# Performance work log

Hardware: AMD Instinct MI355X
Metric: run time of the kernel (lower is better)

The kernel has to match this reference:

```python
import jax, jax.numpy as jnp
import numpy as np

B, N, H = 4, 256, 128
T = 8  # triplet hidden width


def _linear_init(key, fan_in, fan_out):
    s = 1.0 / np.sqrt(fan_in)
    kw, kb = jax.random.split(key)
    W = jax.random.uniform(kw, (fan_in, fan_out), minval=-s, maxval=s, dtype=jnp.float32)
    b = jax.random.uniform(kb, (fan_out,), minval=-s, maxval=s, dtype=jnp.float32)
    return W, b


def setup_inputs() -> dict:
    key = jax.random.key(0)
    ks = jax.random.split(key, 16)
    inp = {
        "node_embeddings": jax.random.normal(ks[0], (B, N, H), dtype=jnp.float32),
        "edge_embeddings": jax.random.normal(ks[1], (B, N, H), dtype=jnp.float32),
        "graph_embeddings": jax.random.normal(ks[2], (B, H), dtype=jnp.float32),
        "previous_hidden": jax.random.normal(ks[3], (B, N, H), dtype=jnp.float32),
    }
    # message MLP: (z_i 2H, z_j 2H, edge_j H, graph H) = 6H -> H -> H -> H
    inp["Wm1"], inp["bm1"] = _linear_init(ks[4], 6 * H, H)
    inp["Wm2"], inp["bm2"] = _linear_init(ks[5], H, H)
    inp["Wm3"], inp["bm3"] = _linear_init(ks[6], H, H)
    # gate MLP: (z 2H, m H, edge H, graph H) = 5H -> H -> H (sigmoid)
    inp["Wg1"], inp["bg1"] = _linear_init(ks[7], 5 * H, H)
    inp["Wg2"], inp["bg2"] = _linear_init(ks[8], H, H)
    # readout: (z 2H, m H) = 3H -> H
    inp["Wr"], inp["br"] = _linear_init(ks[9], 3 * H, H)
    # triplet MLP: (node_j H, node_k H, node H, edge 3H, graph H) = 7H -> 8 (relu)
    inp["Wt1"], inp["bt1"] = _linear_init(ks[10], 7 * H, T)
    # triplet edge readout: 8 -> H
    inp["Wt2"], inp["bt2"] = _linear_init(ks[11], T, H)
    # layer norm params
    inp["gamma"] = jnp.ones((H,), dtype=jnp.float32)
    inp["beta"] = jnp.zeros((H,), dtype=jnp.float32)
    return inp


def reference(node_embeddings, edge_embeddings, graph_embeddings, previous_hidden,
              Wm1, bm1, Wm2, bm2, Wm3, bm3,
              Wg1, bg1, Wg2, bg2, Wr, br,
              Wt1, bt1, Wt2, bt2, gamma, beta):
    h = node_embeddings.shape[-1]
    z = jnp.concatenate([node_embeddings, previous_hidden], axis=-1)  # [B,N,2H]

    # ---- pairwise messages: decompose first linear so the 6H-wide concat is never built ----
    W_zi, W_zj = Wm1[: 2 * h], Wm1[2 * h: 4 * h]
    W_e, W_g = Wm1[4 * h: 5 * h], Wm1[5 * h:]
    u = z @ W_zi + (graph_embeddings @ W_g)[:, None, :] + bm1   # per-i part [B,N,H]
    v = z @ W_zj + edge_embeddings @ W_e                        # per-j part [B,N,H]
    h1 = jax.nn.relu(u[:, :, None, :] + v[:, None, :, :])       # [B,Ni,Nj,H]
    h2 = jax.nn.relu(h1 @ Wm2 + bm2)
    msgs = h2 @ Wm3 + bm3                                       # [B,Ni,Nj,H]
    m = jnp.max(msgs, axis=2)                                   # max over j -> [B,N,H]

    gb = jnp.broadcast_to(graph_embeddings[:, None, :], node_embeddings.shape)
    gate_in = jnp.concatenate([z, m, edge_embeddings, gb], axis=-1)  # [B,N,5H]
    g = jax.nn.sigmoid(jax.nn.relu(gate_in @ Wg1 + bg1) @ Wg2 + bg2)
    h_i = jnp.concatenate([z, m], axis=-1) @ Wr + br
    h_g = g * h_i + (1.0 - g) * previous_hidden

    # ---- triplet messages ----
    # pre-activation is separable over (j, k, i), so max over the N^2 (k,j) pairs
    # equals per-channel max_j + max_k (relu is monotone, max commutes with it).
    Wt_j, Wt_k, Wt_n = Wt1[:h], Wt1[h: 2 * h], Wt1[2 * h: 3 * h]
    Wt_e = Wt1[3 * h: 4 * h] + Wt1[4 * h: 5 * h] + Wt1[5 * h: 6 * h]
    Wt_g = Wt1[6 * h:]
    a_j = node_embeddings @ Wt_j   # [B,N,8]
    a_k = node_embeddings @ Wt_k   # [B,N,8]
    c = node_embeddings @ Wt_n + edge_embeddings @ Wt_e + (graph_embeddings @ Wt_g)[:, None, :] + bt1
    t_max = jax.nn.relu(c + jnp.max(a_j, axis=1, keepdims=True) + jnp.max(a_k, axis=1, keepdims=True))
    h_ij = t_max @ Wt2 + bt2       # [B,N,H]

    # ---- layer norm on gated hidden ----
    mu = jnp.mean(h_g, axis=-1, keepdims=True)
    var = jnp.mean(jnp.square(h_g - mu), axis=-1, keepdims=True)
    h_norm = (h_g - mu) * jax.lax.rsqrt(var + 1e-5) * gamma + beta
    return (h_norm, h_ij)
```

## Files before the change

### kernel.cpp

```cpp
#include <hip/hip_runtime.h>
#include <hip/hip_bf16.h>

typedef unsigned short u16;
typedef float f32x4 __attribute__((ext_vector_type(4)));
typedef short s16x8 __attribute__((ext_vector_type(8)));

#define MFMA16(a,b,c) __builtin_amdgcn_mfma_f32_16x16x32_bf16((a),(b),(c),0,0,0)

static __device__ __forceinline__ u16 f2bf(float x){
  union { __hip_bfloat16 b; u16 u; } c;
  c.b = __float2bfloat16(x);
  return c.u;
}

__global__ void prep_kernel(const float* __restrict__ Wm1, const float* __restrict__ Wm2,
                            const float* __restrict__ Wm3, const float* __restrict__ Wg1,
                            const float* __restrict__ Wr,  const float* __restrict__ Wt1,
                            const float* __restrict__ node,const float* __restrict__ prev,
                            const float* __restrict__ edge,const float* __restrict__ graph,
                            u16* __restrict__ WbT, u16* __restrict__ WgrT,
                            u16* __restrict__ Wm2T, u16* __restrict__ Wm3T,
                            u16* __restrict__ gin)
{
  int idx = blockIdx.x * 256 + threadIdx.x;
  if (idx < 147456) {
    int n = idx >> 9, k = idx & 511;
    int part = k >> 7, kk = k & 127;
    float v = 0.f;
    if (n < 128) {
      if (part == 0)      v = Wm1[kk*128 + n];
      else if (part == 1) v = Wm1[(128+kk)*128 + n];
      else if (part == 3) v = Wm1[(640+kk)*128 + n];
    } else if (n < 256) {
      int nn = n - 128;
      if (part == 0)      v = Wm1[(256+kk)*128 + nn];
      else if (part == 1) v = Wm1[(384+kk)*128 + nn];
      else if (part == 2) v = Wm1[(512+kk)*128 + nn];
    } else if (n < 280) {
      int tt = n - 256;
      if (tt < 8)       { if (part == 0) v = Wt1[kk*8 + tt]; }
      else if (tt < 16) { if (part == 0) v = Wt1[(128+kk)*8 + (tt-8)]; }
      else {
        int t = tt - 16;
        if (part == 0)      v = Wt1[(256+kk)*8 + t];
        else if (part == 2) v = Wt1[(384+kk)*8 + t] + Wt1[(512+kk)*8 + t] + Wt1[(640+kk)*8 + t];
        else if (part == 3) v = Wt1[(768+kk)*8 + t];
      }
    }
    WbT[idx] = f2bf(v);
    return;
  }
  idx -= 147456;
  if (idx < 163840) {
    int n = idx / 640, k = idx - n*640;
    int part = k >> 7, kk = k & 127;
    float v = 0.f;
    if (n < 128) {
      int r = (part==0) ? kk : (part==1) ? (128+kk) : (part==2) ? (384+kk)
                        : (part==3) ? (512+kk) : (256+kk);
      v = Wg1[r*128 + n];
    } else {
      int nn = n - 128;
      if (part == 0)      v = Wr[kk*128 + nn];
      else if (part == 1) v = Wr[(128+kk)*128 + nn];
      else if (part == 4) v = Wr[(256+kk)*128 + nn];
    }
    WgrT[idx] = f2bf(v);
    return;
  }
  idx -= 163840;
  if (idx < 16384) { int n = idx >> 7, k = idx & 127; Wm2T[idx] = f2bf(Wm2[k*128 + n]); return; }
  idx -= 16384;
  if (idx < 16384) { int n = idx >> 7, k = idx & 127; Wm3T[idx] = f2bf(Wm3[k*128 + n]); return; }
  idx -= 16384;
  {
    int row = idx >> 9, k = idx & 511;
    int part = k >> 7, kk = k & 127;
    float v;
    if (part == 0)      v = node[row*128 + kk];
    else if (part == 1) v = prev[row*128 + kk];
    else if (part == 2) v = edge[row*128 + kk];
    else                v = graph[(row >> 8)*128 + kk];
    gin[row*640 + k] = f2bf(v);
  }
}

__global__ void gemm_uvt_kernel(const u16* __restrict__ gin, const u16* __restrict__ WbT,
                                float* __restrict__ uvt)
{
  int m0 = blockIdx.x * 16, n0 = blockIdx.y * 16;
  int lane = threadIdx.x;
  int lrow = lane & 15, lgrp = lane >> 4;
  const u16* arow = gin + (size_t)(m0 + lrow) * 640;
  const u16* brow = WbT + (size_t)(n0 + lrow) * 512;
  f32x4 acc = {0.f, 0.f, 0.f, 0.f};
#pragma unroll
  for (int k0 = 0; k0 < 16; ++k0) {
    s16x8 a = *reinterpret_cast<const s16x8*>(arow + k0*32 + lgrp*8);
    s16x8 b = *reinterpret_cast<const s16x8*>(brow + k0*32 + lgrp*8);
    acc = MFMA16(a, b, acc);
  }
#pragma unroll
  for (int r = 0; r < 4; ++r)
    uvt[(size_t)(m0 + lgrp*4 + r) * 288 + n0 + lrow] = acc[r];
}

__global__ void maxat_kernel(const float* __restrict__ uvt, float* __restrict__ mjk)
{
  int b = blockIdx.x;
  int tid = threadIdx.x;
  int row = b*256 + tid;
  __shared__ float part[4][16];
  float v[16];
#pragma unroll
  for (int t = 0; t < 16; ++t) v[t] = uvt[(size_t)row*288 + 256 + t];
#pragma unroll
  for (int off = 32; off >= 1; off >>= 1) {
#pragma unroll
    for (int t = 0; t < 16; ++t) v[t] = fmaxf(v[t], __shfl_xor(v[t], off));
  }
  int wid = tid >> 6;
  if ((tid & 63) == 0) {
#pragma unroll
    for (int t = 0; t < 16; ++t) part[wid][t] = v[t];
  }
  __syncthreads();
  if (tid < 16)
    mjk[b*16 + tid] = fmaxf(fmaxf(part[0][tid], part[1][tid]),
                            fmaxf(part[2][tid], part[3][tid]));
}

__global__ __launch_bounds__(256) void msgmax_kernel(const float* __restrict__ uvt,
    const u16* __restrict__ Wm2T, const u16* __restrict__ Wm3T,
    const float* __restrict__ bm1, const float* __restrict__ bm2,
    const float* __restrict__ bm3, u16* __restrict__ gin)
{
  int bx = blockIdx.x;
  int b  = bx >> 8;
  int tid = threadIdx.x;
  int wave = tid >> 6, lane = tid & 63;
  int lrow = lane & 15, lgrp = lane >> 4;
  int wcol = wave * 32;

  __shared__ float vtile[16][132];
  __shared__ u16   h2t[16][136];

  s16x8 wb2[4][2], wb3[4][2];
#pragma unroll
  for (int n0 = 0; n0 < 2; ++n0) {
    int col = wcol + n0*16 + lrow;
#pragma unroll
    for (int k0 = 0; k0 < 4; ++k0) {
      wb2[k0][n0] = *reinterpret_cast<const s16x8*>(Wm2T + col*128 + k0*32 + lgrp*8);
      wb3[k0][n0] = *reinterpret_cast<const s16x8*>(Wm3T + col*128 + k0*32 + lgrp*8);
    }
  }

  float uf[4][8];
  const float* urow = uvt + (size_t)bx * 288;
#pragma unroll
  for (int k0 = 0; k0 < 4; ++k0) {
    int off = k0*32 + lgrp*8;
    float4 x = *reinterpret_cast<const float4*>(urow + off);
    float4 y = *reinterpret_cast<const float4*>(urow + off + 4);
    float4 p = *reinterpret_cast<const float4*>(bm1 + off);
    float4 q = *reinterpret_cast<const float4*>(bm1 + off + 4);
    uf[k0][0]=x.x+p.x; uf[k0][1]=x.y+p.y; uf[k0][2]=x.z+p.z; uf[k0][3]=x.w+p.w;
    uf[k0][4]=y.x+q.x; uf[k0][5]=y.y+q.y; uf[k0][6]=y.z+q.z; uf[k0][7]=y.w+q.w;
  }
  float bm2v[2], bm3v[2];
#pragma unroll
  for (int n0 = 0; n0 < 2; ++n0) {
    bm2v[n0] = bm2[wcol + n0*16 + lrow];
    bm3v[n0] = bm3[wcol + n0*16 + lrow];
  }

  float mmax[2][4];
#pragma unroll
  for (int n0 = 0; n0 < 2; ++n0)
#pragma unroll
    for (int r = 0; r < 4; ++r) mmax[n0][r] = -1e30f;

  const float* vbase = uvt + (size_t)(b*256) * 288 + 128;
  int sr = tid >> 4, sc = (tid & 15) * 8;

  for (int jt = 0; jt < 16; ++jt) {
    {
      const float* src = vbase + (size_t)(jt*16 + sr) * 288 + sc;
      float4 x = *reinterpret_cast<const float4*>(src);
      float4 y = *reinterpret_cast<const float4*>(src + 4);
      *reinterpret_cast<float4*>(&vtile[sr][sc])   = x;
      *reinterpret_cast<float4*>(&vtile[sr][sc+4]) = y;
    }
    __syncthreads();

    s16x8 a1[4];
#pragma unroll
    for (int k0 = 0; k0 < 4; ++k0) {
      const float* vp = &vtile[lrow][k0*32 + lgrp*8];
      float4 x = *reinterpret_cast<const float4*>(vp);
      float4 y = *reinterpret_cast<const float4*>(vp + 4);
      s16x8 f;
      f[0] = (short)f2bf(fmaxf(uf[k0][0] + x.x, 0.f));
      f[1] = (short)f2bf(fmaxf(uf[k0][1] + x.y, 0.f));
      f[2] = (short)f2bf(fmaxf(uf[k0][2] + x.z, 0.f));
      f[3] = (short)f2bf(fmaxf(uf[k0][3] + x.w, 0.f));
      f[4] = (short)f2bf(fmaxf(uf[k0][4] + y.x, 0.f));
      f[5] = (short)f2bf(fmaxf(uf[k0][5] + y.y, 0.f));
      f[6] = (short)f2bf(fmaxf(uf[k0][6] + y.z, 0.f));
      f[7] = (short)f2bf(fmaxf(uf[k0][7] + y.w, 0.f));
      a1[k0] = f;
    }

    f32x4 acc1[2] = {{0.f,0.f,0.f,0.f},{0.f,0.f,0.f,0.f}};
#pragma unroll
    for (int k0 = 0; k0 < 4; ++k0) {
      acc1[0] = MFMA16(a1[k0], wb2[k0][0], acc1[0]);
      acc1[1] = MFMA16(a1[k0], wb2[k0][1], acc1[1]);
    }

#pragma unroll
    for (int n0 = 0; n0 < 2; ++n0) {
#pragma unroll
      for (int r = 0; r < 4; ++r) {
        float hv = fmaxf(acc1[n0][r] + bm2v[n0], 0.f);
        h2t[lgrp*4 + r][wcol + n0*16 + lrow] = f2bf(hv);
      }
    }
    __syncthreads();

    s16x8 a2[4];
#pragma unroll
    for (int k0 = 0; k0 < 4; ++k0)
      a2[k0] = *reinterpret_cast<const s16x8*>(&h2t[lrow][k0*32 + lgrp*8]);

    f32x4 acc2[2] = {{0.f,0.f,0.f,0.f},{0.f,0.f,0.f,0.f}};
#pragma unroll
    for (int k0 = 0; k0 < 4; ++k0) {
      acc2[0] = MFMA16(a2[k0], wb3[k0][0], acc2[0]);
      acc2[1] = MFMA16(a2[k0], wb3[k0][1], acc2[1]);
    }
#pragma unroll
    for (int n0 = 0; n0 < 2; ++n0)
#pragma unroll
      for (int r = 0; r < 4; ++r)
        mmax[n0][r] = fmaxf(mmax[n0][r], acc2[n0][r] + bm3v[n0]);
  }

#pragma unroll
  for (int n0 = 0; n0 < 2; ++n0) {
    float m = fmaxf(fmaxf(mmax[n0][0], mmax[n0][1]), fmaxf(mmax[n0][2], mmax[n0][3]));
    m = fmaxf(m, __shfl_xor(m, 16));
    m = fmaxf(m, __shfl_xor(m, 32));
    if (lane < 16)
      gin[(size_t)bx*640 + 512 + wcol + n0*16 + lane] = f2bf(m);
  }
}

__global__ void gemm_gate_kernel(const u16* __restrict__ gin, const u16* __restrict__ WgrT,
                                 const float* __restrict__ bg1, const float* __restrict__ br,
                                 float* __restrict__ r1, float* __restrict__ hi)
{
  int m0 = blockIdx.x * 16, n0 = blockIdx.y * 16;
  int lane = threadIdx.x;
  int lrow = lane & 15, lgrp = lane >> 4;
  const u16* arow = gin  + (size_t)(m0 + lrow) * 640;
  const u16* brow = WgrT + (size_t)(n0 + lrow) * 640;
  f32x4 acc = {0.f, 0.f, 0.f, 0.f};
#pragma unroll
  for (int k0 = 0; k0 < 20; ++k0) {
    s16x8 a = *reinterpret_cast<const s16x8*>(arow + k0*32 + lgrp*8);
    s16x8 b = *reinterpret_cast<const s16x8*>(brow + k0*32 + lgrp*8);
    acc = MFMA16(a, b, acc);
  }
  int col = n0 + lrow;
  float bv = (col < 128) ? bg1[col] : br[col - 128];
#pragma unroll
  for (int r = 0; r < 4; ++r) {
    int gr = m0 + lgrp*4 + r;
    if (col < 128) r1[gr*128 + col] = fmaxf(acc[r] + bv, 0.f);
    else           hi[gr*128 + col - 128] = acc[r] + bv;
  }
}

__global__ void finalize_kernel(const float* __restrict__ r1, const float* __restrict__ hi,
                                const float* __restrict__ prev, const float* __restrict__ uvt,
                                const float* __restrict__ mjk,
                                const float* __restrict__ Wg2, const float* __restrict__ bg2,
                                const float* __restrict__ bt1, const float* __restrict__ Wt2,
                                const float* __restrict__ bt2, const float* __restrict__ gamma,
                                const float* __restrict__ beta, float* __restrict__ out)
{
  int row = blockIdx.x;
  int h = threadIdx.x;
  int b = row >> 8;
  __shared__ float r1s[128];
  __shared__ float red[4];
  r1s[h] = r1[row*128 + h];
  __syncthreads();
  float glin = bg2[h];
#pragma unroll 8
  for (int k = 0; k < 128; ++k) glin += r1s[k] * Wg2[k*128 + h];
  float g = 1.f / (1.f + __expf(-glin));
  float hg = g * hi[row*128 + h] + (1.f - g) * prev[row*128 + h];

  float s1 = hg, s2 = hg*hg;
#pragma unroll
  for (int off = 1; off < 64; off <<= 1) {
    s1 += __shfl_xor(s1, off);
    s2 += __shfl_xor(s2, off);
  }
  int wid = h >> 6;
  if ((h & 63) == 0) { red[wid] = s1; red[2 + wid] = s2; }
  __syncthreads();
  float mu  = (red[0] + red[1]) * 0.0078125f;
  float ex2 = (red[2] + red[3]) * 0.0078125f;
  float var = ex2 - mu*mu;
  float hn = (hg - mu) * rsqrtf(var + 1e-5f) * gamma[h] + beta[h];
  out[row*128 + h] = hn;

  float o2 = bt2[h];
#pragma unroll
  for (int t = 0; t < 8; ++t) {
    float tv = uvt[(size_t)row*288 + 272 + t] + bt1[t] + mjk[b*16 + t] + mjk[b*16 + 8 + t];
    tv = fmaxf(tv, 0.f);
    o2 += tv * Wt2[t*128 + h];
  }
  out[131072 + row*128 + h] = o2;
}

extern "C" void kernel_launch(void* const* d_in, const int* in_sizes, int n_in,
                              void* d_out, int out_size, void* d_ws, size_t ws_size,
                              hipStream_t stream) {
  const float* node  = (const float*)d_in[0];
  const float* edge  = (const float*)d_in[1];
  const float* graph = (const float*)d_in[2];
  const float* prev  = (const float*)d_in[3];
  const float* Wm1 = (const float*)d_in[4];
  const float* bm1 = (const float*)d_in[5];
  const float* Wm2 = (const float*)d_in[6];
  const float* bm2 = (const float*)d_in[7];
  const float* Wm3 = (const float*)d_in[8];
  const float* bm3 = (const float*)d_in[9];
  const float* Wg1 = (const float*)d_in[10];
  const float* bg1 = (const float*)d_in[11];
  const float* Wg2 = (const float*)d_in[12];
  const float* bg2 = (const float*)d_in[13];
  const float* Wr  = (const float*)d_in[14];
  const float* br  = (const float*)d_in[15];
  const float* Wt1 = (const float*)d_in[16];
  const float* bt1 = (const float*)d_in[17];
  const float* Wt2 = (const float*)d_in[18];
  const float* bt2 = (const float*)d_in[19];
  const float* gamma = (const float*)d_in[20];
  const float* beta  = (const float*)d_in[21];
  float* out = (float*)d_out;

  char* ws = (char*)d_ws;
  u16*   WbT  = (u16*)(ws + 0);
  u16*   WgrT = (u16*)(ws + 294912);
  u16*   Wm2T = (u16*)(ws + 622592);
  u16*   Wm3T = (u16*)(ws + 655360);
  u16*   gin  = (u16*)(ws + 688128);
  float* uvt  = (float*)(ws + 1998848);
  float* r1   = (float*)(ws + 3178496);
  float* hi   = (float*)(ws + 3702784);
  float* mjk  = (float*)(ws + 4227072);

  prep_kernel<<<3392, 256, 0, stream>>>(Wm1, Wm2, Wm3, Wg1, Wr, Wt1,
                                        node, prev, edge, graph,
                                        WbT, WgrT, Wm2T, Wm3T, gin);
  gemm_uvt_kernel<<<dim3(64, 18), 64, 0, stream>>>(gin, WbT, uvt);
  maxat_kernel<<<4, 256, 0, stream>>>(uvt, mjk);
  msgmax_kernel<<<1024, 256, 0, stream>>>(uvt, Wm2T, Wm3T, bm1, bm2, bm3, gin);
  gemm_gate_kernel<<<dim3(64, 16), 64, 0, stream>>>(gin, WgrT, bg1, br, r1, hi);
  finalize_kernel<<<1024, 128, 0, stream>>>(r1, hi, prev, uvt, mjk,
                                            Wg2, bg2, bt1, Wt2, bt2, gamma, beta, out);
}
```

Before: 71.13 us.

## Restructure message-max kernel: 32-row j tiles, register prefetch, transposed MFMA

The pairwise message/max kernel now handles 32 j rows per iteration, two 16-row sub-tiles, instead of 16. This halves the barrier-separated iterations. The next tile of v is prefetched into registers while the current one is processed. Each wave computes the relu(u+v) bf16 activations for its own 32-column K slice and writes them packed into shared memory, rather than every wave recomputing all 128 columns from an fp32 LDS tile. The MFMA operands are swapped so that the outputs are transposed, which allows packed bf16 stores of h2. The bm3 bias is now added once after the max reduction instead of on every iteration. The changes cost more registers and a longer cross-lane shuffle reduction at the end.

```diff
diff --git a/kernel.cpp b/kernel.cpp
--- a/kernel.cpp
+++ b/kernel.cpp
@@ -2,6 +2,7 @@
 #include <hip/hip_bf16.h>
 
 typedef unsigned short u16;
+typedef unsigned int u32;
 typedef float f32x4 __attribute__((ext_vector_type(4)));
 typedef short s16x8 __attribute__((ext_vector_type(8)));
 
@@ -135,125 +136,134 @@
     const float* __restrict__ bm1, const float* __restrict__ bm2,
     const float* __restrict__ bm3, u16* __restrict__ gin)
 {
-  int bx = blockIdx.x;
-  int b  = bx >> 8;
-  int tid = threadIdx.x;
-  int wave = tid >> 6, lane = tid & 63;
-  int lrow = lane & 15, lgrp = lane >> 4;
-  int wcol = wave * 32;
-
-  __shared__ float vtile[16][132];
-  __shared__ u16   h2t[16][136];
+  const int row = blockIdx.x;
+  const int b   = row >> 8;
+  const int tid = threadIdx.x;
+  const int w   = tid >> 6;
+  const int lane = tid & 63;
+  const int c = lane & 15, g = lane >> 4;
+
+  __shared__ u16 a1s[2][4][16][32];
+  __shared__ u16 h2s[2][16][136];
 
   s16x8 wb2[4][2], wb3[4][2];
 #pragma unroll
-  for (int n0 = 0; n0 < 2; ++n0) {
-    int col = wcol + n0*16 + lrow;
+  for (int mt = 0; mt < 2; ++mt) {
+    int col = w*32 + mt*16 + c;
 #pragma unroll
     for (int k0 = 0; k0 < 4; ++k0) {
-      wb2[k0][n0] = *reinterpret_cast<const s16x8*>(Wm2T + col*128 + k0*32 + lgrp*8);
-      wb3[k0][n0] = *reinterpret_cast<const s16x8*>(Wm3T + col*128 + k0*32 + lgrp*8);
-    }
-  }
-
-  float uf[4][8];
-  const float* urow = uvt + (size_t)bx * 288;
-#pragma unroll
-  for (int k0 = 0; k0 < 4; ++k0) {
-    int off = k0*32 + lgrp*8;
+      wb2[k0][mt] = *reinterpret_cast<const s16x8*>(Wm2T + col*128 + k0*32 + g*8);
+      wb3[k0][mt] = *reinterpret_cast<const s16x8*>(Wm3T + col*128 + k0*32 + g*8);
+    }
+  }
+  float4 bm2v[2];
+#pragma unroll
+  for (int mt = 0; mt < 2; ++mt)
+    bm2v[mt] = *reinterpret_cast<const float4*>(bm2 + w*32 + mt*16 + 4*g);
+
+  const float* urow = uvt + (size_t)row * 288;
+  float uf[8];
+  {
+    int off = w*32 + g*8;
     float4 x = *reinterpret_cast<const float4*>(urow + off);
     float4 y = *reinterpret_cast<const float4*>(urow + off + 4);
     float4 p = *reinterpret_cast<const float4*>(bm1 + off);
     float4 q = *reinterpret_cast<const float4*>(bm1 + off + 4);
-    uf[k0][0]=x.x+p.x; uf[k0][1]=x.y+p.y; uf[k0][2]=x.z+p.z; uf[k0][3]=x.w+p.w;
-    uf[k0][4]=y.x+q.x; uf[k0][5]=y.y+q.y; uf[k0][6]=y.z+q.z; uf[k0][7]=y.w+q.w;
-  }
-  float bm2v[2], bm3v[2];
-#pragma unroll
-  for (int n0 = 0; n0 < 2; ++n0) {
-    bm2v[n0] = bm2[wcol + n0*16 + lrow];
-    bm3v[n0] = bm3[wcol + n0*16 + lrow];
-  }
-
-  float mmax[2][4];
-#pragma unroll
-  for (int n0 = 0; n0 < 2; ++n0)
-#pragma unroll
-    for (int r = 0; r < 4; ++r) mmax[n0][r] = -1e30f;
-
-  const float* vbase = uvt + (size_t)(b*256) * 288 + 128;
-  int sr = tid >> 4, sc = (tid & 15) * 8;
-
-  for (int jt = 0; jt < 16; ++jt) {
-    {
-      const float* src = vbase + (size_t)(jt*16 + sr) * 288 + sc;
-      float4 x = *reinterpret_cast<const float4*>(src);
-      float4 y = *reinterpret_cast<const float4*>(src + 4);
-      *reinterpret_cast<float4*>(&vtile[sr][sc])   = x;
-      *reinterpret_cast<float4*>(&vtile[sr][sc+4]) = y;
-    }
+    uf[0]=x.x+p.x; uf[1]=x.y+p.y; uf[2]=x.z+p.z; uf[3]=x.w+p.w;
+    uf[4]=y.x+q.x; uf[5]=y.y+q.y; uf[6]=y.z+q.z; uf[7]=y.w+q.w;
+  }
+
+  const float* vb = uvt + (size_t)(b*256) * 288 + 128;
+  f32x4 mmax[2];
+#pragma unroll
+  for (int mt = 0; mt < 2; ++mt)
+#pragma unroll
+    for (int r = 0; r < 4; ++r) mmax[mt][r] = -1e30f;
+
+  float4 vc[2][2];
+#define LOADV(IT) do { \
+  _Pragma("unroll") \
+  for (int t = 0; t < 2; ++t) { \
+    const float* p_ = vb + (size_t)((IT)*32 + t*16 + c) * 288 + w*32 + g*8; \
+    vc[t][0] = *reinterpret_cast<const float4*>(p_); \
+    vc[t][1] = *reinterpret_cast<const float4*>(p_ + 4); } } while (0)
+
+  LOADV(0);
+
+  for (int it = 0; it < 8; ++it) {
+#pragma unroll
+    for (int t = 0; t < 2; ++t) {
+      u32 d0 = (u32)f2bf(fmaxf(uf[0] + vc[t][0].x, 0.f))
+             | ((u32)f2bf(fmaxf(uf[1] + vc[t][0].y, 0.f)) << 16);
+      u32 d1 = (u32)f2bf(fmaxf(uf[2] + vc[t][0].z, 0.f))
+             | ((u32)f2bf(fmaxf(uf[3] + vc[t][0].w, 0.f)) << 16);
+      u32 d2 = (u32)f2bf(fmaxf(uf[4] + vc[t][1].x, 0.f))
+             | ((u32)f2bf(fmaxf(uf[5] + vc[t][1].y, 0.f)) << 16);
+      u32 d3 = (u32)f2bf(fmaxf(uf[6] + vc[t][1].z, 0.f))
+             | ((u32)f2bf(fmaxf(uf[7] + vc[t][1].w, 0.f)) << 16);
+      uint4 pk = {d0, d1, d2, d3};
+      *reinterpret_cast<uint4*>(&a1s[t][w][c][g*8]) = pk;
+    }
+    if (it < 7) LOADV(it + 1);
     __syncthreads();
 
-    s16x8 a1[4];
-#pragma unroll
-    for (int k0 = 0; k0 < 4; ++k0) {
-      const float* vp = &vtile[lrow][k0*32 + lgrp*8];
-      float4 x = *reinterpret_cast<const float4*>(vp);
-      float4 y = *reinterpret_cast<const float4*>(vp + 4);
-      s16x8 f;
-      f[0] = (short)f2bf(fmaxf(uf[k0][0] + x.x, 0.f));
-      f[1] = (short)f2bf(fmaxf(uf[k0][1] + x.y, 0.f));
-      f[2] = (short)f2bf(fmaxf(uf[k0][2] + x.z, 0.f));
-      f[3] = (short)f2bf(fmaxf(uf[k0][3] + x.w, 0.f));
-      f[4] = (short)f2bf(fmaxf(uf[k0][4] + y.x, 0.f));
-      f[5] = (short)f2bf(fmaxf(uf[k0][5] + y.y, 0.f));
-      f[6] = (short)f2bf(fmaxf(uf[k0][6] + y.z, 0.f));
-      f[7] = (short)f2bf(fmaxf(uf[k0][7] + y.w, 0.f));
-      a1[k0] = f;
-    }
-
-    f32x4 acc1[2] = {{0.f,0.f,0.f,0.f},{0.f,0.f,0.f,0.f}};
-#pragma unroll
-    for (int k0 = 0; k0 < 4; ++k0) {
-      acc1[0] = MFMA16(a1[k0], wb2[k0][0], acc1[0]);
-      acc1[1] = MFMA16(a1[k0], wb2[k0][1], acc1[1]);
-    }
-
-#pragma unroll
-    for (int n0 = 0; n0 < 2; ++n0) {
-#pragma unroll
-      for (int r = 0; r < 4; ++r) {
-        float hv = fmaxf(acc1[n0][r] + bm2v[n0], 0.f);
-        h2t[lgrp*4 + r][wcol + n0*16 + lrow] = f2bf(hv);
+    f32x4 acc1[2][2] = {{{0,0,0,0},{0,0,0,0}},{{0,0,0,0},{0,0,0,0}}};
+#pragma unroll
+    for (int t = 0; t < 2; ++t)
+#pragma unroll
+      for (int k0 = 0; k0 < 4; ++k0) {
+        s16x8 af = *reinterpret_cast<const s16x8*>(&a1s[t][k0][c][g*8]);
+        acc1[t][0] = MFMA16(wb2[k0][0], af, acc1[t][0]);
+        acc1[t][1] = MFMA16(wb2[k0][1], af, acc1[t][1]);
       }
-    }
+
+#pragma unroll
+    for (int t = 0; t < 2; ++t)
+#pragma unroll
+      for (int mt = 0; mt < 2; ++mt) {
+        u32 lo = (u32)f2bf(fmaxf(acc1[t][mt][0] + bm2v[mt].x, 0.f))
+               | ((u32)f2bf(fmaxf(acc1[t][mt][1] + bm2v[mt].y, 0.f)) << 16);
+        u32 hi = (u32)f2bf(fmaxf(acc1[t][mt][2] + bm2v[mt].z, 0.f))
+               | ((u32)f2bf(fmaxf(acc1[t][mt][3] + bm2v[mt].w, 0.f)) << 16);
+        uint2 pk = {lo, hi};
+        *reinterpret_cast<uint2*>(&h2s[t][c][w*32 + mt*16 + 4*g]) = pk;
+      }
     __syncthreads();
 
-    s16x8 a2[4];
-#pragma unroll
-    for (int k0 = 0; k0 < 4; ++k0)
-      a2[k0] = *reinterpret_cast<const s16x8*>(&h2t[lrow][k0*32 + lgrp*8]);
-
-    f32x4 acc2[2] = {{0.f,0.f,0.f,0.f},{0.f,0.f,0.f,0.f}};
-#pragma unroll
-    for (int k0 = 0; k0 < 4; ++k0) {
-      acc2[0] = MFMA16(a2[k0], wb3[k0][0], acc2[0]);
-      acc2[1] = MFMA16(a2[k0], wb3[k0][1], acc2[1]);
-    }
-#pragma unroll
-    for (int n0 = 0; n0 < 2; ++n0)
+    f32x4 acc2[2][2] = {{{0,0,0,0},{0,0,0,0}},{{0,0,0,0},{0,0,0,0}}};
+#pragma unroll
+    for (int t = 0; t < 2; ++t)
+#pragma unroll
+      for (int k0 = 0; k0 < 4; ++k0) {
+        s16x8 a2 = *reinterpret_cast<const s16x8*>(&h2s[t][c][k0*32 + g*8]);
+        acc2[t][0] = MFMA16(wb3[k0][0], a2, acc2[t][0]);
+        acc2[t][1] = MFMA16(wb3[k0][1], a2, acc2[t][1]);
+      }
+#pragma unroll
+    for (int mt = 0; mt < 2; ++mt)
 #pragma unroll
       for (int r = 0; r < 4; ++r)
-        mmax[n0][r] = fmaxf(mmax[n0][r], acc2[n0][r] + bm3v[n0]);
-  }
-
-#pragma unroll
-  for (int n0 = 0; n0 < 2; ++n0) {
-    float m = fmaxf(fmaxf(mmax[n0][0], mmax[n0][1]), fmaxf(mmax[n0][2], mmax[n0][3]));
-    m = fmaxf(m, __shfl_xor(m, 16));
-    m = fmaxf(m, __shfl_xor(m, 32));
-    if (lane < 16)
-      gin[(size_t)bx*640 + 512 + wcol + n0*16 + lane] = f2bf(m);
+        mmax[mt][r] = fmaxf(mmax[mt][r], fmaxf(acc2[0][mt][r], acc2[1][mt][r]));
+  }
+#undef LOADV
+
+#pragma unroll
+  for (int mt = 0; mt < 2; ++mt) {
+    f32x4 m = mmax[mt];
+#pragma unroll
+    for (int off = 1; off < 16; off <<= 1) {
+      m[0] = fmaxf(m[0], __shfl_xor(m[0], off));
+      m[1] = fmaxf(m[1], __shfl_xor(m[1], off));
+      m[2] = fmaxf(m[2], __shfl_xor(m[2], off));
+      m[3] = fmaxf(m[3], __shfl_xor(m[3], off));
+    }
+    if (c == 0) {
+      int col = w*32 + mt*16 + 4*g;
+      u32 lo = (u32)f2bf(m[0] + bm3[col])   | ((u32)f2bf(m[1] + bm3[col+1]) << 16);
+      u32 hi = (u32)f2bf(m[2] + bm3[col+2]) | ((u32)f2bf(m[3] + bm3[col+3]) << 16);
+      uint2 pk = {lo, hi};
+      *reinterpret_cast<uint2*>(gin + (size_t)row*640 + 512 + col) = pk;
+    }
   }
 }
 
```

Result: faster. 61.21 us (-13.9%).
